# Kernel optimization log

Measured on AMD Instinct MI355X. Metric: run time of the kernel, lower is better.

The kernel has to match this reference:

```python
import jax, jax.numpy as jnp
import numpy as np

H, I, E, K = 1024, 2816, 8, 2  # hidden, intermediate, n_experts, topk
B, S = 2, 2048


def setup_inputs() -> dict:
    key = jax.random.key(0)
    ks = jax.random.split(key, 6)
    def init(k, shape, fan_in):
        return (jax.random.normal(k, shape, jnp.float32) / np.sqrt(fan_in)).astype(jnp.float32)
    return {
        "x": jax.random.normal(ks[0], (B, S, H), jnp.float32),
        "Wgate": init(ks[1], (H, E), H),   # gating Linear weight (in,out layout)
        "bgate": jnp.zeros((E,), jnp.float32),  # gating Linear bias (nn.Linear default bias=True)
        "Wg": init(ks[2], (E, H, I), H),   # stacked gate_proj, mlp_bias=False
        "Wu": init(ks[3], (E, H, I), H),   # stacked up_proj
        "Wd": init(ks[4], (E, I, H), I),   # stacked down_proj
    }


def reference(x, Wgate, bgate, Wg, Wu, Wd):
    Bb, Ss, Hd = x.shape
    xf = x.reshape(-1, Hd)                       # [N, H] flattened tokens
    logits = xf @ Wgate + bgate                  # [N, E] gate logits
    topv, topi = jax.lax.top_k(logits, K)        # [N, K]
    N = xf.shape[0]
    # sparse combine weights: raw top-k LOGITS (no softmax), zeros elsewhere
    # (faithful to torch: scatter of logits_topk into -inf mask; -inf slots
    #  are never read since only selected experts contribute)
    combine = jnp.zeros_like(logits).at[jnp.arange(N)[:, None], topi].set(topv)  # [N, E]
    # dense grouped SwiGLU over all experts, then sparse combine
    g = jnp.einsum('nh,ehi->nei', xf, Wg)        # [N, E, I]
    u = jnp.einsum('nh,ehi->nei', xf, Wu)        # [N, E, I]
    h = jax.nn.silu(g) * u                       # [N, E, I]
    eo = jnp.einsum('nei,eih->neh', h, Wd)       # [N, E, H]
    out = jnp.einsum('neh,ne->nh', eo, combine).reshape(Bb, Ss, Hd)
    return out, logits
```

## Files before the change

### kernel.cpp

```cpp
#include <hip/hip_runtime.h>

#define HDIM 1024
#define IDIM 2816
#define NEXP 8
#define NTOK 4096
#define NROWS 8192
#define RPAD 8320
#define MAXT 71
#define GU_NYT 44
#define GU_TG 8
#define GU_NTG 9
#define GU_NWG (GU_NTG * GU_NYT * GU_TG)
#define DN_KS 2
#define DN_NWG (MAXT * 8 * DN_KS)
#define TLDP 130

typedef short bf16x8 __attribute__((ext_vector_type(8)));
typedef float f32x4 __attribute__((ext_vector_type(4)));
typedef unsigned short u16x8 __attribute__((ext_vector_type(8)));

static __device__ __forceinline__ unsigned short f2bf(float f) {
    union { float f; unsigned int i; } v; v.f = f;
    return (unsigned short)((v.i + 0x7fffu + ((v.i >> 16) & 1u)) >> 16);
}

static __device__ __forceinline__ void gload16(const void* g, void* l) {
    __builtin_amdgcn_global_load_lds(
        (const __attribute__((address_space(1))) unsigned int*)g,
        (__attribute__((address_space(3))) unsigned int*)l, 16, 0, 0);
}

__global__ __launch_bounds__(256) void gating_kernel(
    const float* __restrict__ x, const float* __restrict__ Wgate,
    const float* __restrict__ bgate, float* __restrict__ logits_out,
    int* __restrict__ counts, int* __restrict__ topi, float* __restrict__ topv)
{
    int wave = (blockIdx.x << 2) + (threadIdx.x >> 6);
    int lane = threadIdx.x & 63;
    if (wave >= NTOK) return;
    const float* xr = x + (size_t)wave * HDIM;

    double acc[NEXP];
#pragma unroll
    for (int e = 0; e < NEXP; ++e) acc[e] = 0.0;
    for (int it = 0; it < HDIM / 64; ++it) {
        int h = lane + (it << 6);
        float xv = xr[h];
        const float* wr = Wgate + (size_t)h * NEXP;
#pragma unroll
        for (int e = 0; e < NEXP; ++e) acc[e] += (double)xv * (double)wr[e];
    }
#pragma unroll
    for (int e = 0; e < NEXP; ++e) {
        double v = acc[e];
        for (int off = 32; off; off >>= 1) v += __shfl_xor(v, off, 64);
        acc[e] = v + (double)bgate[e];
    }
    float lf[NEXP];
#pragma unroll
    for (int e = 0; e < NEXP; ++e) lf[e] = (float)acc[e];

    if (lane < NEXP) logits_out[(size_t)wave * NEXP + lane] = lf[lane];

    if (lane == 0) {
        int i1 = 0; float v1 = lf[0];
#pragma unroll
        for (int e = 1; e < NEXP; ++e) if (lf[e] > v1) { v1 = lf[e]; i1 = e; }
        int i2 = -1; float v2 = -3.0e38f;
#pragma unroll
        for (int e = 0; e < NEXP; ++e) {
            if (e == i1) continue;
            if (lf[e] > v2) { v2 = lf[e]; i2 = e; }
        }
        topi[wave * 2 + 0] = i1; topv[wave * 2 + 0] = v1;
        topi[wave * 2 + 1] = i2; topv[wave * 2 + 1] = v2;
        atomicAdd(&counts[i1], 1);
        atomicAdd(&counts[i2], 1);
    }
}

__global__ void offsets_kernel(const int* __restrict__ counts,
                               int* __restrict__ offs, int* __restrict__ cursor,
                               int* __restrict__ ntile, int* __restrict__ te,
                               int* __restrict__ tm0)
{
    if (threadIdx.x == 0 && blockIdx.x == 0) {
        int s = 0;
        for (int e = 0; e < NEXP; ++e) { offs[e] = s; cursor[e] = s; s += counts[e]; }
        offs[NEXP] = s;
        int nt = 0;
        for (int e = 0; e < NEXP; ++e) {
            int c = counts[e], base = offs[e];
            for (int mt = 0; mt * 128 < c; ++mt) { te[nt] = e; tm0[nt] = base + mt * 128; ++nt; }
        }
        *ntile = nt;
    }
}

__global__ __launch_bounds__(256) void scatter_kernel(
    const float* __restrict__ x, const int* __restrict__ topi,
    const float* __restrict__ topv, int* __restrict__ cursor,
    float* __restrict__ row_w, int* __restrict__ tok_of,
    unsigned short* __restrict__ Xg)
{
    int p = (blockIdx.x << 2) + (threadIdx.x >> 6);
    int lane = threadIdx.x & 63;
    if (p >= NROWS) return;
    int n = p >> 1;
    int e = topi[p];
    float w = topv[p];
    int pos = 0;
    if (lane == 0) {
        pos = atomicAdd(&cursor[e], 1);
        row_w[pos] = w;
        tok_of[pos] = n;
    }
    pos = __shfl(pos, 0, 64);
    const float* xr = x + (size_t)n * HDIM;
    unsigned short* dst = Xg + (size_t)pos * HDIM;
#pragma unroll
    for (int it = 0; it < HDIM / 256; ++it) {
        int idx = (it * 64 + lane) * 4;
        float4 v = *reinterpret_cast<const float4*>(&xr[idx]);
        ushort4 o;
        o.x = f2bf(v.x); o.y = f2bf(v.y); o.z = f2bf(v.z); o.w = f2bf(v.w);
        *reinterpret_cast<ushort4*>(&dst[idx]) = o;
    }
}

__global__ __launch_bounds__(256) void transpose_gu_kernel(
    const float* __restrict__ Wg, const float* __restrict__ Wu,
    unsigned short* __restrict__ W2)
{
    __shared__ unsigned short lds[128 * TLDP];
    const int kind = blockIdx.z;
    const int e = blockIdx.y;
    const int tt = blockIdx.x;
    const int tr = tt / 22, tc = tt % 22;
    const int tid = threadIdx.x;

    const float* s0 = (kind ? Wu : Wg) + (size_t)e * HDIM * IDIM;
    {
        int r = tid >> 1, ch = (tid & 1) * 64;
        const float* sp = s0 + (size_t)(tr * 128 + r) * IDIM + tc * 128 + ch;
        unsigned short* lp = &lds[r * TLDP + ch];
#pragma unroll
        for (int q = 0; q < 8; ++q) {
            float4 a = *reinterpret_cast<const float4*>(sp + q * 8);
            float4 b = *reinterpret_cast<const float4*>(sp + q * 8 + 4);
            u16x8 o;
            o[0] = f2bf(a.x); o[1] = f2bf(a.y); o[2] = f2bf(a.z); o[3] = f2bf(a.w);
            o[4] = f2bf(b.x); o[5] = f2bf(b.y); o[6] = f2bf(b.z); o[7] = f2bf(b.w);
            *reinterpret_cast<u16x8*>(lp + q * 8) = o;
        }
    }
    __syncthreads();
    {
        const int g = tid & 15;
        unsigned short* d0 = W2 + (size_t)e * 2 * IDIM * HDIM + tr * 128 + g * 8;
#pragma unroll
        for (int cb = 0; cb < 8; ++cb) {
            int c = cb * 16 + (tid >> 4);
            u16x8 o;
#pragma unroll
            for (int jj = 0; jj < 8; ++jj) o[jj] = lds[(g * 8 + jj) * TLDP + c];
            int i = tc * 128 + c;
            int r2 = ((i >> 4) << 5) + (kind << 4) + (i & 15);
            *reinterpret_cast<u16x8*>(d0 + (size_t)r2 * HDIM) = o;
        }
    }
}

__global__ __launch_bounds__(256) void transpose_d_kernel(
    const float* __restrict__ Wd, unsigned short* __restrict__ Wdt)
{
    __shared__ unsigned short lds[128 * TLDP];
    const int e = blockIdx.y;
    const int tt = blockIdx.x;
    const int tr = tt / 8, tc = tt % 8;
    const int tid = threadIdx.x;

    const float* s0 = Wd + (size_t)e * IDIM * HDIM;
    {
        int r = tid >> 1, ch = (tid & 1) * 64;
        const float* sp = s0 + (size_t)(tr * 128 + r) * HDIM + tc * 128 + ch;
        unsigned short* lp = &lds[r * TLDP + ch];
#pragma unroll
        for (int q = 0; q < 8; ++q) {
            float4 a = *reinterpret_cast<const float4*>(sp + q * 8);
            float4 b = *reinterpret_cast<const float4*>(sp + q * 8 + 4);
            u16x8 o;
            o[0] = f2bf(a.x); o[1] = f2bf(a.y); o[2] = f2bf(a.z); o[3] = f2bf(a.w);
            o[4] = f2bf(b.x); o[5] = f2bf(b.y); o[6] = f2bf(b.z); o[7] = f2bf(b.w);
            *reinterpret_cast<u16x8*>(lp + q * 8) = o;
        }
    }
    __syncthreads();
    {
        const int g = tid & 15;
        unsigned short* d0 = Wdt + (size_t)e * HDIM * IDIM + tr * 128 + g * 8;
#pragma unroll
        for (int cb = 0; cb < 8; ++cb) {
            int c = cb * 16 + (tid >> 4);
            u16x8 o;
#pragma unroll
            for (int jj = 0; jj < 8; ++jj) o[jj] = lds[(g * 8 + jj) * TLDP + c];
            *reinterpret_cast<u16x8*>(d0 + (size_t)(tc * 128 + c) * IDIM) = o;
        }
    }
}

__global__ __launch_bounds__(256, 4) void gateup_kernel(
    const unsigned short* __restrict__ Xg,
    const unsigned short* __restrict__ W2,
    const int* __restrict__ offs,
    const int* __restrict__ ntile, const int* __restrict__ te,
    const int* __restrict__ tm0, unsigned short* __restrict__ hbuf)
{
    __shared__ unsigned short As[128 * 64];
    __shared__ unsigned short Bs[128 * 64];

    int bid = blockIdx.x;
    int xcd = bid & 7, rest = bid >> 3;
    int wg = xcd * (GU_NWG / 8) + rest;
    int tg = wg / (GU_NYT * GU_TG);
    int r2 = wg % (GU_NYT * GU_TG);
    int ny = r2 >> 3, ti = r2 & 7;
    int t = tg * GU_TG + ti;
    if (t >= *ntile) return;

    const int e = te[t];
    const int m0 = tm0[t];
    const int r1 = offs[e + 1];
    const int n0 = ny * 128;

    const unsigned short* wb = W2 + (size_t)e * 2 * IDIM * HDIM;

    const int tid = threadIdx.x;
    const int lane = tid & 63, wv = tid >> 6;
    const int wr = (wv >> 1) * 64, wc = (wv & 1) * 64;
    const int lr = lane & 15, kq16 = lane >> 4;

    const int a_row8 = tid >> 3;
    const int a_c16 = tid & 7;

    f32x4 zero = {0.f, 0.f, 0.f, 0.f};
    f32x4 acc[4][4];
#pragma unroll
    for (int m = 0; m < 4; ++m)
#pragma unroll
        for (int n = 0; n < 4; ++n) acc[m][n] = zero;

    for (int k0 = 0; k0 < HDIM; k0 += 64) {
        __syncthreads();
#pragma unroll
        for (int ch = 0; ch < 4; ++ch) {
            int row = ch * 32 + a_row8;
            int c16s = a_c16 ^ (row & 7);
            gload16(&Xg[(size_t)(m0 + row) * HDIM + k0 + c16s * 8], &As[ch * 2048 + tid * 8]);
            gload16(&wb[(size_t)(n0 + row) * HDIM + k0 + c16s * 8], &Bs[ch * 2048 + tid * 8]);
        }
        __syncthreads();

#pragma unroll
        for (int ks = 0; ks < 2; ++ks) {
            bf16x8 af[4], bf[4];
#pragma unroll
            for (int m = 0; m < 4; ++m) {
                int row = wr + m * 16 + lr;
                int sw = (ks * 4 + kq16) ^ (row & 7);
                af[m] = *reinterpret_cast<const bf16x8*>(&As[row * 64 + sw * 8]);
            }
#pragma unroll
            for (int n = 0; n < 4; ++n) {
                int row = wc + n * 16 + lr;
                int sw = (ks * 4 + kq16) ^ (row & 7);
                bf[n] = *reinterpret_cast<const bf16x8*>(&Bs[row * 64 + sw * 8]);
            }
#pragma unroll
            for (int m = 0; m < 4; ++m)
#pragma unroll
                for (int n = 0; n < 4; ++n)
                    acc[m][n] = __builtin_amdgcn_mfma_f32_16x16x32_bf16(af[m], bf[n], acc[m][n], 0, 0, 0);
        }
    }

    const int rr = (lane >> 4) * 4;
    const int iloc0 = ((wc >> 5) << 4) + lr;
    const int col0 = ny * 64 + iloc0;
#pragma unroll
    for (int m = 0; m < 4; ++m) {
#pragma unroll
        for (int j = 0; j < 4; ++j) {
            int grow = m0 + wr + m * 16 + rr + j;
            if (grow < r1) {
                unsigned short* hr = &hbuf[(size_t)grow * IDIM + col0];
                float g0 = acc[m][0][j], u0 = acc[m][1][j];
                float g1 = acc[m][2][j], u1 = acc[m][3][j];
                hr[0]  = f2bf(g0 / (1.0f + __expf(-g0)) * u0);
                hr[16] = f2bf(g1 / (1.0f + __expf(-g1)) * u1);
            }
        }
    }
}

__global__ __launch_bounds__(256, 4) void down_kernel(
    const unsigned short* __restrict__ hbuf,
    const unsigned short* __restrict__ Wdt,
    const int* __restrict__ offs,
    const int* __restrict__ ntile, const int* __restrict__ te,
    const int* __restrict__ tm0,
    const float* __restrict__ row_w, const int* __restrict__ tok_of,
    float* __restrict__ out)
{
    __shared__ unsigned short As[128 * 64];
    __shared__ unsigned short Bs[128 * 64];

    int bid = blockIdx.x;
    int xcd = bid & 7, rest = bid >> 3;
    int wg = xcd * (DN_NWG / 8) + rest;
    int t = wg >> 4;
    int r = wg & 15;
    int ny = r >> 1;
    int kh = r & 1;
    if (t >= *ntile) return;

    const int e = te[t];
    const int m0 = tm0[t];
    const int r1 = offs[e + 1];
    const int n0 = ny * 128;

    const unsigned short* wd = Wdt + (size_t)e * HDIM * IDIM;

    const int tid = threadIdx.x;
    const int lane = tid & 63, wv = tid >> 6;
    const int wr = (wv >> 1) * 64, wc = (wv & 1) * 64;
    const int lr = lane & 15, kq16 = lane >> 4;

    const int a_row8 = tid >> 3;
    const int a_c16 = tid & 7;

    f32x4 zero = {0.f, 0.f, 0.f, 0.f};
    f32x4 acc[4][4];
#pragma unroll
    for (int m = 0; m < 4; ++m)
#pragma unroll
        for (int n = 0; n < 4; ++n) acc[m][n] = zero;

    const int kbeg = kh * (IDIM / DN_KS);
    const int kend = kbeg + (IDIM / DN_KS);
    for (int k0 = kbeg; k0 < kend; k0 += 64) {
        __syncthreads();
#pragma unroll
        for (int ch = 0; ch < 4; ++ch) {
            int row = ch * 32 + a_row8;
            int c16s = a_c16 ^ (row & 7);
            gload16(&hbuf[(size_t)(m0 + row) * IDIM + k0 + c16s * 8], &As[ch * 2048 + tid * 8]);
            gload16(&wd[(size_t)(n0 + row) * IDIM + k0 + c16s * 8], &Bs[ch * 2048 + tid * 8]);
        }
        __syncthreads();

#pragma unroll
        for (int ks = 0; ks < 2; ++ks) {
            bf16x8 af[4], bf[4];
#pragma unroll
            for (int m = 0; m < 4; ++m) {
                int row = wr + m * 16 + lr;
                int sw = (ks * 4 + kq16) ^ (row & 7);
                af[m] = *reinterpret_cast<const bf16x8*>(&As[row * 64 + sw * 8]);
            }
#pragma unroll
            for (int n = 0; n < 4; ++n) {
                int row = wc + n * 16 + lr;
                int sw = (ks * 4 + kq16) ^ (row & 7);
                bf[n] = *reinterpret_cast<const bf16x8*>(&Bs[row * 64 + sw * 8]);
            }
#pragma unroll
            for (int m = 0; m < 4; ++m)
#pragma unroll
                for (int n = 0; n < 4; ++n)
                    acc[m][n] = __builtin_amdgcn_mfma_f32_16x16x32_bf16(af[m], bf[n], acc[m][n], 0, 0, 0);
        }
    }

    const int rr = (lane >> 4) * 4;
#pragma unroll
    for (int m = 0; m < 4; ++m) {
#pragma unroll
        for (int j = 0; j < 4; ++j) {
            int grow = m0 + wr + m * 16 + rr + j;
            if (grow < r1) {
                float w = row_w[grow];
                int tok = tok_of[grow];
                float* orow = out + (size_t)tok * HDIM + n0 + wc + lr;
#pragma unroll
                for (int n = 0; n < 4; ++n)
                    atomicAdd(&orow[n * 16], acc[m][n][j] * w);
            }
        }
    }
}

extern "C" void kernel_launch(void* const* d_in, const int* in_sizes, int n_in,
                              void* d_out, int out_size, void* d_ws, size_t ws_size,
                              hipStream_t stream)
{
    const float* x     = (const float*)d_in[0];
    const float* Wgate = (const float*)d_in[1];
    const float* bgate = (const float*)d_in[2];
    const float* Wg    = (const float*)d_in[3];
    const float* Wu    = (const float*)d_in[4];
    const float* Wd    = (const float*)d_in[5];
    float* out = (float*)d_out;
    float* logits = out + (size_t)NTOK * HDIM;

    char* ws = (char*)d_ws;
    unsigned short* Xg   = (unsigned short*)ws;
    unsigned short* hbuf = (unsigned short*)(ws + 17039360);
    unsigned short* W2   = (unsigned short*)(ws + 63897600);
    char* meta = ws + 156172288;
    int*   counts = (int*)(meta);
    int*   offs   = (int*)(meta + 64);
    int*   cursor = (int*)(meta + 128);
    int*   ntile  = (int*)(meta + 192);
    int*   te     = (int*)(meta + 256);
    int*   tm0    = (int*)(meta + 768);
    int*   topi   = (int*)(meta + 2048);
    float* topv   = (float*)(meta + 34816);
    float* row_w  = (float*)(meta + 67584);
    int*   tok_of = (int*)(meta + 100352);

    hipMemsetAsync(counts, 0, 32, stream);
    hipMemsetAsync(out, 0, (size_t)NTOK * HDIM * sizeof(float), stream);

    gating_kernel<<<NTOK / 4, 256, 0, stream>>>(x, Wgate, bgate, logits, counts, topi, topv);
    offsets_kernel<<<1, 64, 0, stream>>>(counts, offs, cursor, ntile, te, tm0);
    scatter_kernel<<<NROWS / 4, 256, 0, stream>>>(x, topi, topv, cursor, row_w, tok_of, Xg);

    transpose_gu_kernel<<<dim3(176, NEXP, 2), 256, 0, stream>>>(Wg, Wu, W2);

    gateup_kernel<<<GU_NWG, 256, 0, stream>>>(Xg, W2, offs, ntile, te, tm0, hbuf);

    transpose_d_kernel<<<dim3(176, NEXP), 256, 0, stream>>>(Wd, W2);

    down_kernel<<<DN_NWG, 256, 0, stream>>>(hbuf, W2, offs, ntile, te, tm0, row_w, tok_of, out);
}
```

Before: 510.7 us.

## Replace atomic down-proj scatter with bf16 expert buffer and gather-combine kernel

The down-projection no longer uses split-K with float atomicAdd into the output. It now runs full-K on 64-row tiles (a new 64-row tile list is built in the offsets kernel), scales each row by its routing weight and writes bf16 results into a per-row expert buffer that reuses the Xg workspace. A new combine kernel gathers each token's two expert rows via pos_of and sums them into the output, which also removes the output memset. This trades atomic contention and the memset for an extra launch, a bf16 round-trip of the expert outputs, and reloading the weight tiles for twice as many M tiles.

```diff
diff --git a/kernel.cpp b/kernel.cpp
--- a/kernel.cpp
+++ b/kernel.cpp
@@ -7,18 +7,21 @@
 #define NROWS 8192
 #define RPAD 8320
 #define MAXT 71
+#define MAXT64 136
 #define GU_NYT 44
 #define GU_TG 8
 #define GU_NTG 9
 #define GU_NWG (GU_NTG * GU_NYT * GU_TG)
-#define DN_KS 2
-#define DN_NWG (MAXT * 8 * DN_KS)
+#define DN_NWG (MAXT64 * 8)
 #define TLDP 130
 
 typedef short bf16x8 __attribute__((ext_vector_type(8)));
 typedef float f32x4 __attribute__((ext_vector_type(4)));
 typedef unsigned short u16x8 __attribute__((ext_vector_type(8)));
 
+static __device__ __forceinline__ float bf2f(unsigned int u) {
+    union { unsigned int i; float f; } v; v.i = u << 16; return v.f;
+}
 static __device__ __forceinline__ unsigned short f2bf(float f) {
     union { float f; unsigned int i; } v; v.f = f;
     return (unsigned short)((v.i + 0x7fffu + ((v.i >> 16) & 1u)) >> 16);
@@ -82,25 +85,29 @@
 __global__ void offsets_kernel(const int* __restrict__ counts,
                                int* __restrict__ offs, int* __restrict__ cursor,
                                int* __restrict__ ntile, int* __restrict__ te,
-                               int* __restrict__ tm0)
+                               int* __restrict__ tm0,
+                               int* __restrict__ ntile64, int* __restrict__ te64,
+                               int* __restrict__ tm64)
 {
     if (threadIdx.x == 0 && blockIdx.x == 0) {
         int s = 0;
         for (int e = 0; e < NEXP; ++e) { offs[e] = s; cursor[e] = s; s += counts[e]; }
         offs[NEXP] = s;
-        int nt = 0;
+        int nt = 0, nt64 = 0;
         for (int e = 0; e < NEXP; ++e) {
             int c = counts[e], base = offs[e];
             for (int mt = 0; mt * 128 < c; ++mt) { te[nt] = e; tm0[nt] = base + mt * 128; ++nt; }
+            for (int mt = 0; mt * 64 < c; ++mt) { te64[nt64] = e; tm64[nt64] = base + mt * 64; ++nt64; }
         }
         *ntile = nt;
+        *ntile64 = nt64;
     }
 }
 
 __global__ __launch_bounds__(256) void scatter_kernel(
     const float* __restrict__ x, const int* __restrict__ topi,
     const float* __restrict__ topv, int* __restrict__ cursor,
-    float* __restrict__ row_w, int* __restrict__ tok_of,
+    float* __restrict__ row_w, int* __restrict__ pos_of,
     unsigned short* __restrict__ Xg)
 {
     int p = (blockIdx.x << 2) + (threadIdx.x >> 6);
@@ -113,7 +120,7 @@
     if (lane == 0) {
         pos = atomicAdd(&cursor[e], 1);
         row_w[pos] = w;
-        tok_of[pos] = n;
+        pos_of[p] = pos;
     }
     pos = __shfl(pos, 0, 64);
     const float* xr = x + (size_t)n * HDIM;
@@ -308,25 +315,23 @@
     const unsigned short* __restrict__ hbuf,
     const unsigned short* __restrict__ Wdt,
     const int* __restrict__ offs,
-    const int* __restrict__ ntile, const int* __restrict__ te,
-    const int* __restrict__ tm0,
-    const float* __restrict__ row_w, const int* __restrict__ tok_of,
-    float* __restrict__ out)
-{
-    __shared__ unsigned short As[128 * 64];
+    const int* __restrict__ ntile64, const int* __restrict__ te64,
+    const int* __restrict__ tm64,
+    const float* __restrict__ row_w,
+    unsigned short* __restrict__ eobuf)
+{
+    __shared__ unsigned short As[64 * 64];
     __shared__ unsigned short Bs[128 * 64];
 
     int bid = blockIdx.x;
     int xcd = bid & 7, rest = bid >> 3;
     int wg = xcd * (DN_NWG / 8) + rest;
-    int t = wg >> 4;
-    int r = wg & 15;
-    int ny = r >> 1;
-    int kh = r & 1;
-    if (t >= *ntile) return;
-
-    const int e = te[t];
-    const int m0 = tm0[t];
+    int t = wg >> 3;
+    int ny = wg & 7;
+    if (t >= *ntile64) return;
+
+    const int e = te64[t];
+    const int m0 = tm64[t];
     const int r1 = offs[e + 1];
     const int n0 = ny * 128;
 
@@ -334,43 +339,46 @@
 
     const int tid = threadIdx.x;
     const int lane = tid & 63, wv = tid >> 6;
-    const int wr = (wv >> 1) * 64, wc = (wv & 1) * 64;
+    const int wc = wv * 32;
     const int lr = lane & 15, kq16 = lane >> 4;
 
     const int a_row8 = tid >> 3;
     const int a_c16 = tid & 7;
 
     f32x4 zero = {0.f, 0.f, 0.f, 0.f};
-    f32x4 acc[4][4];
+    f32x4 acc[4][2];
 #pragma unroll
     for (int m = 0; m < 4; ++m)
 #pragma unroll
-        for (int n = 0; n < 4; ++n) acc[m][n] = zero;
-
-    const int kbeg = kh * (IDIM / DN_KS);
-    const int kend = kbeg + (IDIM / DN_KS);
-    for (int k0 = kbeg; k0 < kend; k0 += 64) {
+        for (int n = 0; n < 2; ++n) acc[m][n] = zero;
+
+    for (int k0 = 0; k0 < IDIM; k0 += 64) {
         __syncthreads();
+#pragma unroll
+        for (int ch = 0; ch < 2; ++ch) {
+            int row = ch * 32 + a_row8;
+            int c16s = a_c16 ^ (row & 7);
+            gload16(&hbuf[(size_t)(m0 + row) * IDIM + k0 + c16s * 8], &As[ch * 2048 + tid * 8]);
+        }
 #pragma unroll
         for (int ch = 0; ch < 4; ++ch) {
             int row = ch * 32 + a_row8;
             int c16s = a_c16 ^ (row & 7);
-            gload16(&hbuf[(size_t)(m0 + row) * IDIM + k0 + c16s * 8], &As[ch * 2048 + tid * 8]);
             gload16(&wd[(size_t)(n0 + row) * IDIM + k0 + c16s * 8], &Bs[ch * 2048 + tid * 8]);
         }
         __syncthreads();
 
 #pragma unroll
         for (int ks = 0; ks < 2; ++ks) {
-            bf16x8 af[4], bf[4];
+            bf16x8 af[4], bf[2];
 #pragma unroll
             for (int m = 0; m < 4; ++m) {
-                int row = wr + m * 16 + lr;
+                int row = m * 16 + lr;
                 int sw = (ks * 4 + kq16) ^ (row & 7);
                 af[m] = *reinterpret_cast<const bf16x8*>(&As[row * 64 + sw * 8]);
             }
 #pragma unroll
-            for (int n = 0; n < 4; ++n) {
+            for (int n = 0; n < 2; ++n) {
                 int row = wc + n * 16 + lr;
                 int sw = (ks * 4 + kq16) ^ (row & 7);
                 bf[n] = *reinterpret_cast<const bf16x8*>(&Bs[row * 64 + sw * 8]);
@@ -378,7 +386,7 @@
 #pragma unroll
             for (int m = 0; m < 4; ++m)
 #pragma unroll
-                for (int n = 0; n < 4; ++n)
+                for (int n = 0; n < 2; ++n)
                     acc[m][n] = __builtin_amdgcn_mfma_f32_16x16x32_bf16(af[m], bf[n], acc[m][n], 0, 0, 0);
         }
     }
@@ -388,17 +396,41 @@
     for (int m = 0; m < 4; ++m) {
 #pragma unroll
         for (int j = 0; j < 4; ++j) {
-            int grow = m0 + wr + m * 16 + rr + j;
+            int grow = m0 + m * 16 + rr + j;
             if (grow < r1) {
                 float w = row_w[grow];
-                int tok = tok_of[grow];
-                float* orow = out + (size_t)tok * HDIM + n0 + wc + lr;
-#pragma unroll
-                for (int n = 0; n < 4; ++n)
-                    atomicAdd(&orow[n * 16], acc[m][n][j] * w);
-            }
-        }
-    }
+                unsigned short* er = &eobuf[(size_t)grow * HDIM + n0 + wc + lr];
+#pragma unroll
+                for (int n = 0; n < 2; ++n)
+                    er[n * 16] = f2bf(acc[m][n][j] * w);
+            }
+        }
+    }
+}
+
+__global__ __launch_bounds__(256) void combine_kernel(
+    const unsigned short* __restrict__ eobuf, const int* __restrict__ pos_of,
+    float* __restrict__ out)
+{
+    int t = blockIdx.x * 256 + threadIdx.x;
+    int n = t >> 7;
+    int c = (t & 127) << 3;
+    int p0 = pos_of[n * 2 + 0];
+    int p1 = pos_of[n * 2 + 1];
+    uint4 a = *reinterpret_cast<const uint4*>(&eobuf[(size_t)p0 * HDIM + c]);
+    uint4 b = *reinterpret_cast<const uint4*>(&eobuf[(size_t)p1 * HDIM + c]);
+    float4 o0, o1;
+    o0.x = bf2f(a.x & 0xffffu) + bf2f(b.x & 0xffffu);
+    o0.y = bf2f(a.x >> 16)     + bf2f(b.x >> 16);
+    o0.z = bf2f(a.y & 0xffffu) + bf2f(b.y & 0xffffu);
+    o0.w = bf2f(a.y >> 16)     + bf2f(b.y >> 16);
+    o1.x = bf2f(a.z & 0xffffu) + bf2f(b.z & 0xffffu);
+    o1.y = bf2f(a.z >> 16)     + bf2f(b.z >> 16);
+    o1.z = bf2f(a.w & 0xffffu) + bf2f(b.w & 0xffffu);
+    o1.w = bf2f(a.w >> 16)     + bf2f(b.w >> 16);
+    float* op = out + (size_t)n * HDIM + c;
+    *reinterpret_cast<float4*>(op) = o0;
+    *reinterpret_cast<float4*>(op + 4) = o1;
 }
 
 extern "C" void kernel_launch(void* const* d_in, const int* in_sizes, int n_in,
@@ -419,23 +451,26 @@
     unsigned short* hbuf = (unsigned short*)(ws + 17039360);
     unsigned short* W2   = (unsigned short*)(ws + 63897600);
     char* meta = ws + 156172288;
-    int*   counts = (int*)(meta);
-    int*   offs   = (int*)(meta + 64);
-    int*   cursor = (int*)(meta + 128);
-    int*   ntile  = (int*)(meta + 192);
-    int*   te     = (int*)(meta + 256);
-    int*   tm0    = (int*)(meta + 768);
-    int*   topi   = (int*)(meta + 2048);
-    float* topv   = (float*)(meta + 34816);
-    float* row_w  = (float*)(meta + 67584);
-    int*   tok_of = (int*)(meta + 100352);
+    int*   counts  = (int*)(meta);
+    int*   offs    = (int*)(meta + 64);
+    int*   cursor  = (int*)(meta + 128);
+    int*   ntile   = (int*)(meta + 192);
+    int*   ntile64 = (int*)(meta + 196);
+    int*   te      = (int*)(meta + 256);
+    int*   tm0     = (int*)(meta + 768);
+    int*   te64    = (int*)(meta + 1280);
+    int*   tm64    = (int*)(meta + 2048);
+    int*   topi    = (int*)(meta + 4096);
+    float* topv    = (float*)(meta + 36864);
+    float* row_w   = (float*)(meta + 69632);
+    int*   pos_of  = (int*)(meta + 102400);
 
     hipMemsetAsync(counts, 0, 32, stream);
-    hipMemsetAsync(out, 0, (size_t)NTOK * HDIM * sizeof(float), stream);
 
     gating_kernel<<<NTOK / 4, 256, 0, stream>>>(x, Wgate, bgate, logits, counts, topi, topv);
-    offsets_kernel<<<1, 64, 0, stream>>>(counts, offs, cursor, ntile, te, tm0);
-    scatter_kernel<<<NROWS / 4, 256, 0, stream>>>(x, topi, topv, cursor, row_w, tok_of, Xg);
+    offsets_kernel<<<1, 64, 0, stream>>>(counts, offs, cursor, ntile, te, tm0,
+                                         ntile64, te64, tm64);
+    scatter_kernel<<<NROWS / 4, 256, 0, stream>>>(x, topi, topv, cursor, row_w, pos_of, Xg);
 
     transpose_gu_kernel<<<dim3(176, NEXP, 2), 256, 0, stream>>>(Wg, Wu, W2);
 
@@ -443,5 +478,8 @@
 
     transpose_d_kernel<<<dim3(176, NEXP), 256, 0, stream>>>(Wd, W2);
 
-    down_kernel<<<DN_NWG, 256, 0, stream>>>(hbuf, W2, offs, ntile, te, tm0, row_w, tok_of, out);
-}
+    down_kernel<<<DN_NWG, 256, 0, stream>>>(hbuf, W2, offs, ntile64, te64, tm64,
+                                            row_w, Xg );
+
+    combine_kernel<<<NTOK * HDIM / 8 / 256, 256, 0, stream>>>(Xg, pos_of, out);
+}
```

Result: faster. 489.4 us (-4.2%).
